# Performance work log

Hardware: AMD Instinct MI355X
Metric: run time of the kernel (lower is better)

## Reference

```python
import jax, jax.numpy as jnp
import numpy as np

D_IN, D_K, D_V = 1024, 128, 128
B, S = 8, 4096


def setup_inputs() -> dict:
    key = jax.random.key(0)
    kq, kk, kv, kwq, kwk, kwv = jax.random.split(key, 6)
    q = jax.random.normal(kq, (B, S, D_IN), dtype=jnp.float32)
    k = jax.random.normal(kk, (B, S, D_IN), dtype=jnp.float32)
    v = jax.random.normal(kv, (B, S, D_IN), dtype=jnp.float32)
    # nn.Linear(d_in, d_out, bias=None): weight shape [d_out, d_in], y = x @ W^T
    scale = 1.0 / np.sqrt(D_IN)
    Wq = jax.random.uniform(kwq, (D_K, D_IN), jnp.float32, -scale, scale)
    Wk = jax.random.uniform(kwk, (D_K, D_IN), jnp.float32, -scale, scale)
    Wv = jax.random.uniform(kwv, (D_V, D_IN), jnp.float32, -scale, scale)
    return {"q": q, "k": k, "v": v, "Wq": Wq, "Wk": Wk, "Wv": Wv}


def reference(q, k, v, Wq, Wk, Wv):
    # Bias-free projections: [b, s, d_in] @ [d_in, d_k/d_v]
    qh = jnp.einsum('bsd,kd->bsk', q, Wq)
    kh = jnp.einsum('bsd,kd->bsk', k, Wk)
    vh = jnp.einsum('bsd,vd->bsv', v, Wv)
    scores = jnp.einsum('bqk,bsk->bqs', qh, kh) / jnp.sqrt(jnp.float32(D_K))
    attn = jax.nn.softmax(scores, axis=-1)  # [b, s_q, s_kv]
    return jnp.einsum('bqs,bsv->bqv', attn, vh)
```

## Files before the change

kernel.cpp:

```cpp
#include <hip/hip_runtime.h>
#include <hip/hip_bf16.h>
#include <stdint.h>

#define D_IN 1024
#define D_K  128
#define NBATCH 8
#define SEQ  4096
#define MROWS (NBATCH * SEQ)

typedef __attribute__((ext_vector_type(8))) short bf16x8;
typedef __attribute__((ext_vector_type(4))) float f32x4;

__device__ __forceinline__ unsigned short f32_to_bf16(float x) {
    union { float f; uint32_t u; } v; v.f = x;
    uint32_t r = 0x7FFFu + ((v.u >> 16) & 1u);
    return (unsigned short)((v.u + r) >> 16);
}

__device__ __forceinline__ bf16x8 cvt8(float4 lo, float4 hi) {
    bf16x8 r;
    r[0] = (short)f32_to_bf16(lo.x); r[1] = (short)f32_to_bf16(lo.y);
    r[2] = (short)f32_to_bf16(lo.z); r[3] = (short)f32_to_bf16(lo.w);
    r[4] = (short)f32_to_bf16(hi.x); r[5] = (short)f32_to_bf16(hi.y);
    r[6] = (short)f32_to_bf16(hi.z); r[7] = (short)f32_to_bf16(hi.w);
    return r;
}

__device__ __forceinline__ void gload16(const void* src, void* lds) {
    __builtin_amdgcn_global_load_lds(
        (const __attribute__((address_space(1))) void*)src,
        (__attribute__((address_space(3))) void*)lds, 16, 0, 0);
}

__global__ __launch_bounds__(256)
void wconv_kernel(const float* __restrict__ Wq, const float* __restrict__ Wk,
                  const float* __restrict__ Wv, unsigned short* __restrict__ Wt)
{
    const int t  = blockIdx.x * 256 + threadIdx.x;
    const int n  = t & 127;
    const int kc = (t >> 7) & 127;
    const int p  = t >> 14;
    const float* __restrict__ W = (p == 0) ? Wq : (p == 1) ? Wk : Wv;
    const float sc = (p == 0) ? (1.44269504088896f * 0.0883883476483184f) : 1.0f;
    const float4* src = reinterpret_cast<const float4*>(W + (size_t)n * D_IN + kc * 8);
    float4 a = src[0], b = src[1];
    uint4 o;
    o.x = (uint32_t)f32_to_bf16(a.x * sc) | ((uint32_t)f32_to_bf16(a.y * sc) << 16);
    o.y = (uint32_t)f32_to_bf16(a.z * sc) | ((uint32_t)f32_to_bf16(a.w * sc) << 16);
    o.z = (uint32_t)f32_to_bf16(b.x * sc) | ((uint32_t)f32_to_bf16(b.y * sc) << 16);
    o.w = (uint32_t)f32_to_bf16(b.z * sc) | ((uint32_t)f32_to_bf16(b.w * sc) << 16);
    *reinterpret_cast<uint4*>(Wt + (size_t)t * 8) = o;
}

#define RBM 32

__global__ __launch_bounds__(256, 2)
void proj_kernel(const float* __restrict__ Xq, const float* __restrict__ Xk,
                 const float* __restrict__ Xv,
                 const unsigned short* __restrict__ Wt,
                 unsigned short* __restrict__ qh, unsigned short* __restrict__ kh,
                 unsigned short* __restrict__ vhT)
{
    const int p = blockIdx.y;
    const float* __restrict__ X = (p == 0) ? Xq : (p == 1) ? Xk : Xv;
    const unsigned short* __restrict__ Wtp = Wt + (size_t)p * 128 * 128 * 8;

    __shared__ unsigned short As[RBM * 1024];
    __shared__ unsigned short Bs[8 * 128 * 8];

    const int tid  = threadIdx.x;
    const int lane = tid & 63;
    const int wave = tid >> 6;
    const int lrow = lane & 15;
    const int g    = lane >> 4;
    const int wr   = (wave >> 1) * 16;
    const int wc   = (wave & 1) * 64;
    const int wbase = blockIdx.x * RBM;

    {
        const int r0 = wave * 8;
        const char* rowp = reinterpret_cast<const char*>(
            X + (size_t)(wbase + r0) * D_IN) + lane * 32;
        float4 a0 = *reinterpret_cast<const float4*>(rowp);
        float4 a1 = *reinterpret_cast<const float4*>(rowp + 16);
        float4 a2 = *reinterpret_cast<const float4*>(rowp + 2048);
        float4 a3 = *reinterpret_cast<const float4*>(rowp + 2048 + 16);
        #pragma unroll
        for (int i = 0; i < 8; ++i) {
            float4 c0 = a0, c1 = a1, c2 = a2, c3 = a3;
            if (i < 7) {
                const char* np = rowp + (size_t)(i + 1) * 4096;
                a0 = *reinterpret_cast<const float4*>(np);
                a1 = *reinterpret_cast<const float4*>(np + 16);
                a2 = *reinterpret_cast<const float4*>(np + 2048);
                a3 = *reinterpret_cast<const float4*>(np + 2048 + 16);
            }
            const int r = r0 + i;
            char* base = reinterpret_cast<char*>(As) + r * 2048;
            const int swz = (r & 7) << 4;
            *reinterpret_cast<bf16x8*>(base + ((lane * 16) ^ swz)) = cvt8(c0, c1);
            *reinterpret_cast<bf16x8*>(base + ((1024 + lane * 16) ^ swz)) = cvt8(c2, c3);
        }
    }

    {
        const uint4* src = reinterpret_cast<const uint4*>(Wtp) + tid * 4;
        #pragma unroll
        for (int j = 0; j < 4; ++j) {
            uint4 v = src[j];
            const int i  = tid * 4 + j;
            const int kc = i >> 7, n = i & 127;
            *reinterpret_cast<uint4*>(reinterpret_cast<char*>(Bs) +
                kc * 2048 + ((n ^ kc) * 16)) = v;
        }
    }
    __syncthreads();

    f32x4 acc[4];
    #pragma unroll
    for (int ni = 0; ni < 4; ++ni) acc[ni] = (f32x4){0.f, 0.f, 0.f, 0.f};

    const int arow = wr + lrow;
    const char* abase = reinterpret_cast<const char*>(As) + arow * 2048;
    const int aswz = (arow & 7) << 4;

    for (int q = 0; q < 16; ++q) {
        uint4 nb0, nb1, nb2, nb3;
        if (q < 15) {
            const uint4* src = reinterpret_cast<const uint4*>(
                Wtp + (size_t)(q + 1) * 8192) + tid * 4;
            nb0 = src[0]; nb1 = src[1]; nb2 = src[2]; nb3 = src[3];
        }

        #pragma unroll
        for (int s = 0; s < 2; ++s) {
            const int t = 2 * q + s;
            const int kcl = s * 4 + g;
            bf16x8 af = *reinterpret_cast<const bf16x8*>(
                abase + ((t * 64 + g * 16) ^ aswz));
            #pragma unroll
            for (int ni = 0; ni < 4; ++ni) {
                const int n = wc + ni * 16 + lrow;
                bf16x8 bf = *reinterpret_cast<const bf16x8*>(
                    reinterpret_cast<const char*>(Bs) + kcl * 2048 + ((n ^ kcl) * 16));
                acc[ni] = __builtin_amdgcn_mfma_f32_16x16x32_bf16(af, bf, acc[ni], 0, 0, 0);
            }
        }

        __syncthreads();
        if (q < 15) {
            #pragma unroll
            for (int j = 0; j < 4; ++j) {
                uint4 v = (j == 0) ? nb0 : (j == 1) ? nb1 : (j == 2) ? nb2 : nb3;
                const int i  = tid * 4 + j;
                const int kc = i >> 7, n = i & 127;
                *reinterpret_cast<uint4*>(reinterpret_cast<char*>(Bs) +
                    kc * 2048 + ((n ^ kc) * 16)) = v;
            }
            __syncthreads();
        }
    }

    if (p < 2) {
        unsigned short* __restrict__ Y = (p == 0) ? qh : kh;
        const int rbase = wbase + wr + g * 4;
        #pragma unroll
        for (int ni = 0; ni < 4; ++ni) {
            const int n = wc + ni * 16 + lrow;
            #pragma unroll
            for (int r = 0; r < 4; ++r)
                Y[(size_t)(rbase + r) * D_K + n] = f32_to_bf16(acc[ni][r]);
        }
    } else {
        const int b  = wbase >> 12;
        const int s  = (wbase & 4095) + wr + g * 4;
        #pragma unroll
        for (int ni = 0; ni < 4; ++ni) {
            const int d = wc + ni * 16 + lrow;
            uint2 t;
            t.x = (uint32_t)f32_to_bf16(acc[ni][0]) |
                  ((uint32_t)f32_to_bf16(acc[ni][1]) << 16);
            t.y = (uint32_t)f32_to_bf16(acc[ni][2]) |
                  ((uint32_t)f32_to_bf16(acc[ni][3]) << 16);
            *reinterpret_cast<uint2*>(vhT + ((size_t)(b * D_K + d) << 12) + s) = t;
        }
    }
}

#define KVB 64

__global__ __launch_bounds__(256, 2)
void attn_kernel(const unsigned short* __restrict__ qh,
                 const unsigned short* __restrict__ kh,
                 const unsigned short* __restrict__ vhT,
                 float* __restrict__ out)
{
    __shared__ unsigned short Ks[2][KVB * D_K];
    __shared__ unsigned short Vs[2][D_K * KVB];
    __shared__ unsigned short Ps[4][16 * KVB];

    const int tid  = threadIdx.x;
    const int lane = tid & 63;
    const int wave = tid >> 6;
    const int b    = blockIdx.x & 7;
    const int qt   = blockIdx.x >> 3;
    const int q0   = qt * 64 + wave * 16;
    const int lrow = lane & 15;
    const int g4   = (lane >> 4) << 2;
    const int lk16 = (lane >> 4) * 16;

    const unsigned short* __restrict__ Kb = kh + (size_t)b * SEQ * D_K;
    const unsigned short* __restrict__ Vb = vhT + (size_t)b * D_K * SEQ;
    unsigned short* const Pw = Ps[wave];

    const int kr0  = lane >> 4;
    const int kcbp = (lane & 15) * 16;
    const int vr0  = lane >> 3;
    const int vcbp = (lane & 7) * 16;

    #define STAGE(buf, it_)                                                   \
    do {                                                                      \
        const int s0_ = (it_) * KVB;                                          \
        _Pragma("unroll")                                                     \
        for (int j = 0; j < 4; ++j) {                                         \
            const int blk  = wave * 4 + j;                                    \
            const int krow = blk * 4 + kr0;                                   \
            gload16(reinterpret_cast<const char*>(Kb) +                       \
                        (size_t)(s0_ + krow) * 256 +                          \
                        (kcbp ^ ((krow & 7) << 4)),                           \
                    reinterpret_cast<char*>(Ks[buf]) + blk * 1024);           \
            const int vrow = blk * 8 + vr0;                                   \
            gload16(reinterpret_cast<const char*>(Vb) +                       \
                        (size_t)vrow * (SEQ * 2) + (size_t)s0_ * 2 +          \
                        (vcbp ^ ((vrow & 7) << 4)),                           \
                    reinterpret_cast<char*>(Vs[buf]) + blk * 1024);           \
        }                                                                     \
    } while (0)

    bf16x8 qf[4];
    {
        const char* base = reinterpret_cast<const char*>(
            qh + (size_t)(b * SEQ + q0 + lrow) * D_K);
        #pragma unroll
        for (int ks = 0; ks < 4; ++ks)
            qf[ks] = *reinterpret_cast<const bf16x8*>(base + ks * 64 + lk16);
    }

    f32x4 o[8];
    #pragma unroll
    for (int df = 0; df < 8; ++df) o[df] = (f32x4){0.f, 0.f, 0.f, 0.f};
    float lsum[4] = {0.f, 0.f, 0.f, 0.f};

    STAGE(0, 0);
    asm volatile("s_waitcnt vmcnt(0)" ::: "memory");
    __syncthreads();

    int cur = 0;
    for (int it = 0; it < SEQ / KVB; ++it) {
        if (it + 1 < SEQ / KVB) STAGE(cur ^ 1, it + 1);

        f32x4 sc[4];
        #pragma unroll
        for (int sf = 0; sf < 4; ++sf) sc[sf] = (f32x4){0.f, 0.f, 0.f, 0.f};
        #pragma unroll
        for (int ks = 0; ks < 4; ++ks) {
            #pragma unroll
            for (int sf = 0; sf < 4; ++sf) {
                const int row = sf * 16 + lrow;
                bf16x8 kf = *reinterpret_cast<const bf16x8*>(
                    reinterpret_cast<const char*>(Ks[cur]) + row * 256 +
                    ((ks * 64 + lk16) ^ ((row & 7) << 4)));
                sc[sf] = __builtin_amdgcn_mfma_f32_16x16x32_bf16(qf[ks], kf, sc[sf], 0, 0, 0);
            }
        }

        #pragma unroll
        for (int sf = 0; sf < 4; ++sf) {
            #pragma unroll
            for (int r = 0; r < 4; ++r) {
                float pv = exp2f(sc[sf][r]);
                lsum[r] += pv;
                const int prow = g4 + r;
                const int pcol = (sf * 16 + lrow) * 2;
                *reinterpret_cast<unsigned short*>(
                    reinterpret_cast<char*>(Pw) + prow * 128 +
                    (pcol ^ ((prow & 7) << 4))) = f32_to_bf16(pv);
            }
        }

        #pragma unroll
        for (int ks = 0; ks < 2; ++ks) {
            bf16x8 pf = *reinterpret_cast<const bf16x8*>(
                reinterpret_cast<const char*>(Pw) + lrow * 128 +
                ((ks * 64 + lk16) ^ ((lrow & 7) << 4)));
            #pragma unroll
            for (int df = 0; df < 8; ++df) {
                const int vr = df * 16 + lrow;
                bf16x8 vf = *reinterpret_cast<const bf16x8*>(
                    reinterpret_cast<const char*>(Vs[cur]) + vr * 128 +
                    ((ks * 64 + lk16) ^ ((vr & 7) << 4)));
                o[df] = __builtin_amdgcn_mfma_f32_16x16x32_bf16(pf, vf, o[df], 0, 0, 0);
            }
        }

        asm volatile("s_waitcnt vmcnt(0)" ::: "memory");
        __syncthreads();
        cur ^= 1;
    }
    #undef STAGE

    #pragma unroll
    for (int r = 0; r < 4; ++r) {
        float s = lsum[r];
        s += __shfl_xor(s, 1);
        s += __shfl_xor(s, 2);
        s += __shfl_xor(s, 4);
        s += __shfl_xor(s, 8);
        float inv = 1.0f / s;
        const int row = q0 + g4 + r;
        float* ob = out + (size_t)(b * SEQ + row) * D_K + lrow;
        #pragma unroll
        for (int df = 0; df < 8; ++df)
            ob[df * 16] = o[df][r] * inv;
    }
}

extern "C" void kernel_launch(void* const* d_in, const int* in_sizes, int n_in,
                              void* d_out, int out_size, void* d_ws, size_t ws_size,
                              hipStream_t stream)
{
    (void)in_sizes; (void)n_in; (void)out_size; (void)ws_size;
    const float* q  = (const float*)d_in[0];
    const float* k  = (const float*)d_in[1];
    const float* v  = (const float*)d_in[2];
    const float* Wq = (const float*)d_in[3];
    const float* Wk = (const float*)d_in[4];
    const float* Wv = (const float*)d_in[5];

    unsigned short* qh  = (unsigned short*)d_ws;
    unsigned short* kh  = qh + (size_t)MROWS * D_K;
    unsigned short* vhT = kh + (size_t)MROWS * D_K;
    unsigned short* Wt  = vhT + (size_t)MROWS * D_K;

    wconv_kernel<<<dim3(192), 256, 0, stream>>>(Wq, Wk, Wv, Wt);
    proj_kernel<<<dim3(MROWS / RBM, 3), 256, 0, stream>>>(q, k, v, Wt, qh, kh, vhT);
    attn_kernel<<<dim3(NBATCH * (SEQ / 64)), 256, 0, stream>>>(qh, kh, vhT, (float*)d_out);
}
```

Before: 240.7 us.

## Load projection weight fragments directly from global into registers, drop LDS staging

```diff
diff --git a/kernel.cpp b/kernel.cpp
--- a/kernel.cpp
+++ b/kernel.cpp
@@ -66,7 +66,6 @@
     const unsigned short* __restrict__ Wtp = Wt + (size_t)p * 128 * 128 * 8;
 
     __shared__ unsigned short As[RBM * 1024];
-    __shared__ unsigned short Bs[8 * 128 * 8];
 
     const int tid  = threadIdx.x;
     const int lane = tid & 63;
@@ -102,18 +101,6 @@
             *reinterpret_cast<bf16x8*>(base + ((1024 + lane * 16) ^ swz)) = cvt8(c2, c3);
         }
     }
-
-    {
-        const uint4* src = reinterpret_cast<const uint4*>(Wtp) + tid * 4;
-        #pragma unroll
-        for (int j = 0; j < 4; ++j) {
-            uint4 v = src[j];
-            const int i  = tid * 4 + j;
-            const int kc = i >> 7, n = i & 127;
-            *reinterpret_cast<uint4*>(reinterpret_cast<char*>(Bs) +
-                kc * 2048 + ((n ^ kc) * 16)) = v;
-        }
-    }
     __syncthreads();
 
     f32x4 acc[4];
@@ -123,41 +110,35 @@
     const int arow = wr + lrow;
     const char* abase = reinterpret_cast<const char*>(As) + arow * 2048;
     const int aswz = (arow & 7) << 4;
-
-    for (int q = 0; q < 16; ++q) {
-        uint4 nb0, nb1, nb2, nb3;
-        if (q < 15) {
-            const uint4* src = reinterpret_cast<const uint4*>(
-                Wtp + (size_t)(q + 1) * 8192) + tid * 4;
-            nb0 = src[0]; nb1 = src[1]; nb2 = src[2]; nb3 = src[3];
-        }
-
-        #pragma unroll
-        for (int s = 0; s < 2; ++s) {
-            const int t = 2 * q + s;
-            const int kcl = s * 4 + g;
+    const unsigned short* __restrict__ wb0 = Wtp + ((size_t)g * 128 + wc + lrow) * 8;
+
+    bf16x8 bb[16];
+
+    #pragma unroll
+    for (int s = 0; s < 4; ++s)
+        #pragma unroll
+        for (int ni = 0; ni < 4; ++ni)
+            bb[s * 4 + ni] = *reinterpret_cast<const bf16x8*>(
+                wb0 + ((size_t)s * 4 * 128 + ni * 16) * 8);
+
+    #pragma unroll
+    for (int bt = 0; bt < 8; ++bt) {
+        #pragma unroll
+        for (int s = 0; s < 4; ++s) {
+            const int t = bt * 4 + s;
             bf16x8 af = *reinterpret_cast<const bf16x8*>(
                 abase + ((t * 64 + g * 16) ^ aswz));
-            #pragma unroll
-            for (int ni = 0; ni < 4; ++ni) {
-                const int n = wc + ni * 16 + lrow;
-                bf16x8 bf = *reinterpret_cast<const bf16x8*>(
-                    reinterpret_cast<const char*>(Bs) + kcl * 2048 + ((n ^ kcl) * 16));
-                acc[ni] = __builtin_amdgcn_mfma_f32_16x16x32_bf16(af, bf, acc[ni], 0, 0, 0);
-            }
-        }
-
-        __syncthreads();
-        if (q < 15) {
-            #pragma unroll
-            for (int j = 0; j < 4; ++j) {
-                uint4 v = (j == 0) ? nb0 : (j == 1) ? nb1 : (j == 2) ? nb2 : nb3;
-                const int i  = tid * 4 + j;
-                const int kc = i >> 7, n = i & 127;
-                *reinterpret_cast<uint4*>(reinterpret_cast<char*>(Bs) +
-                    kc * 2048 + ((n ^ kc) * 16)) = v;
-            }
-            __syncthreads();
+            acc[0] = __builtin_amdgcn_mfma_f32_16x16x32_bf16(af, bb[s * 4 + 0], acc[0], 0, 0, 0);
+            acc[1] = __builtin_amdgcn_mfma_f32_16x16x32_bf16(af, bb[s * 4 + 1], acc[1], 0, 0, 0);
+            acc[2] = __builtin_amdgcn_mfma_f32_16x16x32_bf16(af, bb[s * 4 + 2], acc[2], 0, 0, 0);
+            acc[3] = __builtin_amdgcn_mfma_f32_16x16x32_bf16(af, bb[s * 4 + 3], acc[3], 0, 0, 0);
+            if (bt < 7) {
+                const size_t kcb = ((size_t)(bt + 1) * 16 + s * 4) * 128 * 8;
+                #pragma unroll
+                for (int ni = 0; ni < 4; ++ni)
+                    bb[s * 4 + ni] = *reinterpret_cast<const bf16x8*>(
+                        wb0 + kcb + (size_t)ni * 16 * 8);
+            }
         }
     }
 
```

New measurement: 226.5 us. 1.06x faster.
